# Kernel optimization log

Measured on AMD Instinct MI355X. Metric: run time of the kernel, lower is better.

## Reference

```python
import jax, jax.numpy as jnp
import numpy as np

B, N, K = 8, 2048, 16
C_IN, C_MID, C_OUT = 64, 16, 64
WH = [32, 32]
FH = [256]


def _mlp_params(key, dims, scale_keyed=True):
    ps = []
    for i in range(len(dims) - 1):
        key, k1 = jax.random.split(key)
        w = jax.random.normal(k1, (dims[i], dims[i + 1]), jnp.float32) / np.sqrt(dims[i])
        b = jnp.zeros((dims[i + 1],), jnp.float32)
        ps += [w, b]
    return ps


def setup_inputs() -> dict:
    key = jax.random.key(0)
    k1, k2, k3, k4, k5 = jax.random.split(key, 5)
    groups = jnp.broadcast_to(jnp.arange(N, dtype=jnp.int32) // K, (B, N))
    points = jax.random.normal(k1, (B, N, 3), jnp.float32)
    feats = jax.random.normal(k2, (B, N, C_IN), jnp.float32)
    point_mask = (jax.random.uniform(k3, (B, N)) > 0.1).astype(jnp.float32)
    w1, b1, w2, b2, w3, b3 = _mlp_params(k4, [3] + WH + [C_MID])
    f1, fb1, f2, fb2 = _mlp_params(k5, [C_IN * C_MID] + FH + [C_OUT])
    return {"groups": groups, "points": points, "feats": feats,
            "point_mask": point_mask,
            "w1": w1, "b1": b1, "w2": w2, "b2": b2, "w3": w3, "b3": b3,
            "f1": f1, "fb1": fb1, "f2": f2, "fb2": fb2}


def _neighbor_idxs(groups):
    # matches[b,i,j] = groups[b,i]==groups[b,j]; torch .nonzero yields, per (b,i),
    # the matching j in increasing order -> stable argsort of ~matches, take first K.
    matches = groups[:, :, None] == groups[:, None, :]            # [B,N,N]
    return jnp.argsort((~matches).astype(jnp.int32), axis=-1)[:, :, :K]  # [B,N,K]


def reference(groups, points, feats, point_mask,
              w1, b1, w2, b2, w3, b3, f1, fb1, f2, fb2):
    idxs = _neighbor_idxs(groups)                                  # [B,N,K] int
    gather = jax.vmap(lambda arr, ix: arr[ix])                     # per-batch gather
    nb_pts = gather(points, idxs)                                  # [B,N,K,3]
    nb_feats = gather(feats, idxs)                                 # [B,N,K,C_IN]
    rel = points[:, :, None, :] - nb_pts                           # [B,N,K,3] (xy encoding = identity)

    # weight_conv: pointwise MLP 3 -> 32 -> 32 -> C_MID, then explicit ReLU
    h = jax.nn.relu(rel @ w1 + b1)
    h = jax.nn.relu(h @ w2 + b2)
    m = jax.nn.relu(h @ w3 + b3)                                   # [B,N,K,C_MID]

    tmask = gather(point_mask, idxs)                               # [B,N,K]
    m = m * tmask[..., None]
    nb_feats = nb_feats * tmask[..., None]

    # per-(point) matmul: [C_MID,K] x [K,C_IN] -> flatten C_MID-major
    e = jnp.einsum('bnkm,bnkc->bnmc', m, nb_feats)                 # [B,N,C_MID,C_IN]
    e = e.reshape(B, N, C_MID * C_IN)

    # final_conv: pointwise MLP 1024 -> 256 -> C_OUT
    h2 = jax.nn.relu(e @ f1 + fb1)
    out = h2 @ f2 + fb2                                            # [B,N,C_OUT]
    return out
```

## Files before the change

kernel.cpp:

```cpp
#include <hip/hip_runtime.h>

typedef unsigned short u16;
typedef short bf16x8 __attribute__((ext_vector_type(8)));
typedef float f32x4  __attribute__((ext_vector_type(4)));
typedef u16   u16x4  __attribute__((ext_vector_type(4)));

__device__ __forceinline__ u16 f2bf(float f) {
  union { float f; unsigned int i; } v; v.f = f;
  unsigned int r = (v.i + 0x7FFFu + ((v.i >> 16) & 1u)) >> 16;
  return (u16)r;
}

__global__ __launch_bounds__(256) void repack_k(const float* __restrict__ f1,
                                                const float* __restrict__ f2,
                                                u16* __restrict__ f1p,
                                                u16* __restrict__ f2p) {
  const int o = blockIdx.x * 256 + threadIdx.x;
  if (o < 262144) {
    const int j = o & 7, n = (o >> 3) & 255, kb = o >> 11;
    f1p[o] = f2bf(f1[(kb * 8 + j) * 256 + n]);
  }
  if (o < 16384) {
    const int j = o & 7, n = (o >> 3) & 63, kb = o >> 9;
    f2p[o] = f2bf(f2[(kb * 8 + j) * 64 + n]);
  }
}

__global__ __launch_bounds__(256) void fused_k(
    const float* __restrict__ points, const float* __restrict__ feats,
    const float* __restrict__ pmask,
    const float* __restrict__ w1, const float* __restrict__ b1,
    const float* __restrict__ w2, const float* __restrict__ b2,
    const float* __restrict__ w3, const float* __restrict__ b3,
    const u16* __restrict__ f1p, const float* __restrict__ fb1,
    const u16* __restrict__ f2p, const float* __restrict__ fb2,
    float* __restrict__ out) {
  const int gi = blockIdx.x;
  const int bb = blockIdx.y;
  const int base = gi * 16;
  const int t = threadIdx.x;

  __shared__ float Wl[1712];
  __shared__ float Pl[16][3];
  __shared__ float Mask[16];
  __shared__ float F[1024];
  __shared__ __align__(16) u16 E[16 * 1032];
  __shared__ __align__(16) union {
    float Ml[16 * 16 * 17];
    u16   H2[16 * 264];
  } U;

  for (int idx = t; idx < 96;   idx += 256) Wl[idx]        = w1[idx];
  for (int idx = t; idx < 32;   idx += 256) Wl[96 + idx]   = b1[idx];
  for (int idx = t; idx < 1024; idx += 256) Wl[128 + idx]  = w2[idx];
  for (int idx = t; idx < 32;   idx += 256) Wl[1152 + idx] = b2[idx];
  for (int idx = t; idx < 512;  idx += 256) Wl[1184 + idx] = w3[idx];
  for (int idx = t; idx < 16;   idx += 256) Wl[1696 + idx] = b3[idx];
  if (t < 16) {
    Mask[t] = pmask[bb * 2048 + base + t];
    const int p = (bb * 2048 + base + t) * 3;
    Pl[t][0] = points[p + 0];
    Pl[t][1] = points[p + 1];
    Pl[t][2] = points[p + 2];
  }
  __syncthreads();

  for (int e = t; e < 1024; e += 256) {
    const int k = e >> 6;
    F[e] = feats[(bb * 2048 + base) * 64 + e] * Mask[k];
  }
  {
    const int i = t >> 4, k = t & 15;
    const float r0 = Pl[i][0] - Pl[k][0];
    const float r1 = Pl[i][1] - Pl[k][1];
    const float r2 = Pl[i][2] - Pl[k][2];
    float h1[32];
#pragma unroll
    for (int o = 0; o < 32; ++o) {
      float a = Wl[96 + o];
      a = fmaf(r0, Wl[o], a);
      a = fmaf(r1, Wl[32 + o], a);
      a = fmaf(r2, Wl[64 + o], a);
      h1[o] = fmaxf(a, 0.f);
    }
    float h2[32];
#pragma unroll
    for (int o = 0; o < 32; ++o) h2[o] = Wl[1152 + o];
#pragma unroll
    for (int j = 0; j < 32; ++j) {
      const float hj = h1[j];
      const float* w = &Wl[128 + j * 32];
#pragma unroll
      for (int o = 0; o < 32; ++o) h2[o] = fmaf(hj, w[o], h2[o]);
    }
#pragma unroll
    for (int o = 0; o < 32; ++o) h2[o] = fmaxf(h2[o], 0.f);
    float mo[16];
#pragma unroll
    for (int o = 0; o < 16; ++o) mo[o] = Wl[1696 + o];
#pragma unroll
    for (int j = 0; j < 32; ++j) {
      const float hj = h2[j];
      const float* w = &Wl[1184 + j * 16];
#pragma unroll
      for (int o = 0; o < 16; ++o) mo[o] = fmaf(hj, w[o], mo[o]);
    }
    const float mk = Mask[k];
    float* Mrow = &U.Ml[(i * 16 + k) * 17];
#pragma unroll
    for (int o = 0; o < 16; ++o) Mrow[o] = fmaxf(mo[o], 0.f) * mk;
  }
  __syncthreads();

  {
    const int i = t >> 4;
    const int c0 = (t & 15) * 4;
    float acc[16][4] = {};
#pragma unroll
    for (int k = 0; k < 16; ++k) {
      const float* Fr = &F[k * 64 + c0];
      const float f0 = Fr[0], fA = Fr[1], fB = Fr[2], fC = Fr[3];
      const float* Mrow = &U.Ml[(i * 16 + k) * 17];
#pragma unroll
      for (int mi = 0; mi < 16; ++mi) {
        const float mv = Mrow[mi];
        acc[mi][0] = fmaf(mv, f0, acc[mi][0]);
        acc[mi][1] = fmaf(mv, fA, acc[mi][1]);
        acc[mi][2] = fmaf(mv, fB, acc[mi][2]);
        acc[mi][3] = fmaf(mv, fC, acc[mi][3]);
      }
    }
    __syncthreads();
#pragma unroll
    for (int mi = 0; mi < 16; ++mi) {
      u16x4 v = { f2bf(acc[mi][0]), f2bf(acc[mi][1]), f2bf(acc[mi][2]), f2bf(acc[mi][3]) };
      *(u16x4*)&E[i * 1032 + mi * 64 + c0] = v;
    }
  }
  __syncthreads();

  {
    const int wv = t >> 6;
    const int lane = t & 63;
    const int q = lane >> 4, r16 = lane & 15;
    const int nb = wv * 64;
    f32x4 acc[4] = {};
    for (int ks = 0; ks < 32; ++ks) {
      const int k0 = ks * 32;
      const bf16x8 a = *(const bf16x8*)&E[r16 * 1032 + k0 + q * 8];
      const int kb = (k0 >> 3) + q;
#pragma unroll
      for (int nt = 0; nt < 4; ++nt) {
        const bf16x8 bv = *(const bf16x8*)&f1p[(kb * 256 + nb + nt * 16 + r16) * 8];
        acc[nt] = __builtin_amdgcn_mfma_f32_16x16x32_bf16(a, bv, acc[nt], 0, 0, 0);
      }
    }
    __syncthreads();
#pragma unroll
    for (int nt = 0; nt < 4; ++nt) {
      const int col = nb + nt * 16 + r16;
      const float bias = fb1[col];
#pragma unroll
      for (int r = 0; r < 4; ++r)
        U.H2[(q * 4 + r) * 264 + col] = f2bf(fmaxf(acc[nt][r] + bias, 0.f));
    }
  }
  __syncthreads();

  {
    const int wv = t >> 6;
    const int lane = t & 63;
    const int q = lane >> 4, r16 = lane & 15;
    const int n0 = wv * 16;
    f32x4 acc = {};
#pragma unroll
    for (int ks = 0; ks < 8; ++ks) {
      const int k0 = ks * 32;
      const bf16x8 a = *(const bf16x8*)&U.H2[r16 * 264 + k0 + q * 8];
      const bf16x8 bv = *(const bf16x8*)&f2p[(((k0 >> 3) + q) * 64 + n0 + r16) * 8];
      acc = __builtin_amdgcn_mfma_f32_16x16x32_bf16(a, bv, acc, 0, 0, 0);
    }
    const int col = n0 + r16;
    const float bias = fb2[col];
#pragma unroll
    for (int r = 0; r < 4; ++r) {
      const int row = q * 4 + r;
      out[((size_t)(bb * 2048 + base + row)) * 64 + col] = acc[r] + bias;
    }
  }
}

extern "C" void kernel_launch(void* const* d_in, const int* in_sizes, int n_in,
                              void* d_out, int out_size, void* d_ws, size_t ws_size,
                              hipStream_t stream) {
  const float* points = (const float*)d_in[1];
  const float* feats  = (const float*)d_in[2];
  const float* pmask  = (const float*)d_in[3];
  const float* w1 = (const float*)d_in[4];
  const float* b1 = (const float*)d_in[5];
  const float* w2 = (const float*)d_in[6];
  const float* b2 = (const float*)d_in[7];
  const float* w3 = (const float*)d_in[8];
  const float* b3 = (const float*)d_in[9];
  const float* f1 = (const float*)d_in[10];
  const float* fb1 = (const float*)d_in[11];
  const float* f2 = (const float*)d_in[12];
  const float* fb2 = (const float*)d_in[13];
  float* out = (float*)d_out;

  u16* f1p = (u16*)d_ws;
  u16* f2p = f1p + 262144;

  repack_k<<<dim3(1024), dim3(256), 0, stream>>>(f1, f2, f1p, f2p);
  fused_k<<<dim3(128, 8), dim3(256), 0, stream>>>(points, feats, pmask,
                                                  w1, b1, w2, b2, w3, b3,
                                                  f1p, fb1, f2p, fb2, out);
}
```

Baseline: 131.7 us.

## Split fused kernel into MLP/einsum stage and tiled double-buffered GEMM

Splits the work into two kernels. The first runs the weight MLP and the einsum, writes E to a global bf16 workspace, and folds in the f1/f2 repacking. The second is a 64-row-tile GEMM that double-buffers A tiles into LDS with XOR swizzling via global_load_lds, then applies the second layer. The aim is more reuse of the f1 weights per block (64 rows instead of 16) and overlapping loads with MFMA, at the cost of a 32MB round trip through global memory for E. It falls back to the old path when the workspace is too small.

```diff
diff --git a/kernel.cpp b/kernel.cpp
--- a/kernel.cpp
+++ b/kernel.cpp
@@ -25,6 +25,227 @@
     f2p[o] = f2bf(f2[(kb * 8 + j) * 64 + n]);
   }
 }
+
+__global__ __launch_bounds__(256) void mlp_einsum_k(
+    const float* __restrict__ points, const float* __restrict__ feats,
+    const float* __restrict__ pmask,
+    const float* __restrict__ w1, const float* __restrict__ b1,
+    const float* __restrict__ w2, const float* __restrict__ b2,
+    const float* __restrict__ w3, const float* __restrict__ b3,
+    const float* __restrict__ f1, const float* __restrict__ f2,
+    u16* __restrict__ f1p, u16* __restrict__ f2p,
+    u16* __restrict__ Eg) {
+  const int gi = blockIdx.x;
+  const int bb = blockIdx.y;
+  const int base = gi * 16;
+  const int t = threadIdx.x;
+
+  __shared__ float Wl[1712];
+  __shared__ float Pl[16][3];
+  __shared__ float Mask[16];
+  __shared__ float F[1024];
+  __shared__ float Ml[16 * 16 * 17];
+
+  {
+    const int o = (bb * 128 + gi) * 256 + t;
+    { const int j = o & 7, n = (o >> 3) & 255, kb = o >> 11;
+      f1p[o] = f2bf(f1[(kb * 8 + j) * 256 + n]); }
+    if (o < 16384) {
+      const int j = o & 7, n = (o >> 3) & 63, kb = o >> 9;
+      f2p[o] = f2bf(f2[(kb * 8 + j) * 64 + n]);
+    }
+  }
+
+  for (int idx = t; idx < 96;   idx += 256) Wl[idx]        = w1[idx];
+  for (int idx = t; idx < 32;   idx += 256) Wl[96 + idx]   = b1[idx];
+  for (int idx = t; idx < 1024; idx += 256) Wl[128 + idx]  = w2[idx];
+  for (int idx = t; idx < 32;   idx += 256) Wl[1152 + idx] = b2[idx];
+  for (int idx = t; idx < 512;  idx += 256) Wl[1184 + idx] = w3[idx];
+  for (int idx = t; idx < 16;   idx += 256) Wl[1696 + idx] = b3[idx];
+  if (t < 16) {
+    Mask[t] = pmask[bb * 2048 + base + t];
+    const int p = (bb * 2048 + base + t) * 3;
+    Pl[t][0] = points[p + 0];
+    Pl[t][1] = points[p + 1];
+    Pl[t][2] = points[p + 2];
+  }
+  __syncthreads();
+
+  for (int e = t; e < 1024; e += 256) {
+    const int k = e >> 6;
+    F[e] = feats[(bb * 2048 + base) * 64 + e] * Mask[k];
+  }
+  {
+    const int i = t >> 4, k = t & 15;
+    const float r0 = Pl[i][0] - Pl[k][0];
+    const float r1 = Pl[i][1] - Pl[k][1];
+    const float r2 = Pl[i][2] - Pl[k][2];
+    float h1[32];
+#pragma unroll
+    for (int o = 0; o < 32; ++o) {
+      float a = Wl[96 + o];
+      a = fmaf(r0, Wl[o], a);
+      a = fmaf(r1, Wl[32 + o], a);
+      a = fmaf(r2, Wl[64 + o], a);
+      h1[o] = fmaxf(a, 0.f);
+    }
+    float h2[32];
+#pragma unroll
+    for (int o = 0; o < 32; ++o) h2[o] = Wl[1152 + o];
+#pragma unroll
+    for (int j = 0; j < 32; ++j) {
+      const float hj = h1[j];
+      const float* w = &Wl[128 + j * 32];
+#pragma unroll
+      for (int o = 0; o < 32; ++o) h2[o] = fmaf(hj, w[o], h2[o]);
+    }
+#pragma unroll
+    for (int o = 0; o < 32; ++o) h2[o] = fmaxf(h2[o], 0.f);
+    float mo[16];
+#pragma unroll
+    for (int o = 0; o < 16; ++o) mo[o] = Wl[1696 + o];
+#pragma unroll
+    for (int j = 0; j < 32; ++j) {
+      const float hj = h2[j];
+      const float* w = &Wl[1184 + j * 16];
+#pragma unroll
+      for (int o = 0; o < 16; ++o) mo[o] = fmaf(hj, w[o], mo[o]);
+    }
+    const float mk = Mask[k];
+    float* Mrow = &Ml[(i * 16 + k) * 17];
+#pragma unroll
+    for (int o = 0; o < 16; ++o) Mrow[o] = fmaxf(mo[o], 0.f) * mk;
+  }
+  __syncthreads();
+
+  {
+    const int i = t >> 4;
+    const int c0 = (t & 15) * 4;
+    float acc[16][4] = {};
+#pragma unroll
+    for (int k = 0; k < 16; ++k) {
+      const float* Fr = &F[k * 64 + c0];
+      const float f0 = Fr[0], fA = Fr[1], fB = Fr[2], fC = Fr[3];
+      const float* Mrow = &Ml[(i * 16 + k) * 17];
+#pragma unroll
+      for (int mi = 0; mi < 16; ++mi) {
+        const float mv = Mrow[mi];
+        acc[mi][0] = fmaf(mv, f0, acc[mi][0]);
+        acc[mi][1] = fmaf(mv, fA, acc[mi][1]);
+        acc[mi][2] = fmaf(mv, fB, acc[mi][2]);
+        acc[mi][3] = fmaf(mv, fC, acc[mi][3]);
+      }
+    }
+    u16* Erow = Eg + (size_t)(bb * 2048 + base + i) * 1024;
+#pragma unroll
+    for (int mi = 0; mi < 16; ++mi) {
+      u16x4 v = { f2bf(acc[mi][0]), f2bf(acc[mi][1]),
+                  f2bf(acc[mi][2]), f2bf(acc[mi][3]) };
+      *(u16x4*)&Erow[mi * 64 + c0] = v;
+    }
+  }
+}
+
+#define STAGE(bf_, kc_)                                                        \
+  do {                                                                         \
+    const int rl_ = lane >> 3;                                       \
+    const int sg_ = (lane & 7) ^ rl_;         \
+    const u16* s0_ =                                                           \
+        Eg + (size_t)(R + wv * 8 + rl_) * 1024 + (kc_) + sg_ * 8;              \
+    u16* d0_ = &Asw[bf_][(wv * 8) * 64];            \
+    u16* d1_ = &Asw[bf_][(32 + wv * 8) * 64];                                  \
+    __builtin_amdgcn_global_load_lds(                                          \
+        (const __attribute__((address_space(1))) void*)s0_,                    \
+        (__attribute__((address_space(3))) void*)d0_, 16, 0, 0);               \
+    __builtin_amdgcn_global_load_lds(                                          \
+        (const __attribute__((address_space(1))) void*)(s0_ + 32 * 1024),      \
+        (__attribute__((address_space(3))) void*)d1_, 16, 0, 0);               \
+  } while (0)
+
+__global__ __launch_bounds__(256) void gemm_k(
+    const u16* __restrict__ Eg, const u16* __restrict__ f1p,
+    const float* __restrict__ fb1, const u16* __restrict__ f2p,
+    const float* __restrict__ fb2, float* __restrict__ out) {
+  const int R = blockIdx.x * 64;
+  const int t = threadIdx.x;
+  const int wv = t >> 6, lane = t & 63;
+  const int q = lane >> 4, r16 = lane & 15;
+
+  __shared__ __align__(16) u16 Asw[2][64 * 64];
+  __shared__ __align__(16) u16 H2[64 * 264];
+
+  const int nb = wv * 64;
+  f32x4 acc[4][4] = {};
+
+  STAGE(0, 0);
+  for (int c = 0; c < 16; ++c) {
+    const int bf = c & 1;
+    asm volatile("s_waitcnt vmcnt(0)" ::: "memory");
+    __builtin_amdgcn_s_barrier();
+
+    bf16x8 bv[2][4];
+#pragma unroll
+    for (int ksl = 0; ksl < 2; ++ksl) {
+      const int kb = c * 8 + ksl * 4 + q;
+#pragma unroll
+      for (int nt = 0; nt < 4; ++nt)
+        bv[ksl][nt] =
+            *(const bf16x8*)&f1p[(size_t)(kb * 256 + nb + nt * 16 + r16) * 8];
+    }
+    bf16x8 a[2][4];
+#pragma unroll
+    for (int ksl = 0; ksl < 2; ++ksl)
+#pragma unroll
+      for (int rt = 0; rt < 4; ++rt) {
+        const int r = rt * 16 + r16;
+        const int g = (ksl * 4 + q) ^ (r & 7);
+        a[ksl][rt] = *(const bf16x8*)&Asw[bf][r * 64 + g * 8];
+      }
+    __builtin_amdgcn_sched_barrier(0);
+    if (c < 15) STAGE(bf ^ 1, (c + 1) * 64);
+    __builtin_amdgcn_sched_barrier(0);
+#pragma unroll
+    for (int ksl = 0; ksl < 2; ++ksl)
+#pragma unroll
+      for (int nt = 0; nt < 4; ++nt)
+#pragma unroll
+        for (int rt = 0; rt < 4; ++rt)
+          acc[rt][nt] = __builtin_amdgcn_mfma_f32_16x16x32_bf16(
+              a[ksl][rt], bv[ksl][nt], acc[rt][nt], 0, 0, 0);
+    __builtin_amdgcn_s_barrier();
+  }
+
+#pragma unroll
+  for (int nt = 0; nt < 4; ++nt) {
+    const int col = nb + nt * 16 + r16;
+    const float bias = fb1[col];
+#pragma unroll
+    for (int rt = 0; rt < 4; ++rt)
+#pragma unroll
+      for (int r = 0; r < 4; ++r)
+        H2[(rt * 16 + q * 4 + r) * 264 + col] =
+            f2bf(fmaxf(acc[rt][nt][r] + bias, 0.f));
+  }
+  __syncthreads();
+
+  const int n0 = wv * 16;
+  const float bias2 = fb2[n0 + r16];
+#pragma unroll
+  for (int rt = 0; rt < 4; ++rt) {
+    f32x4 a2 = {};
+#pragma unroll
+    for (int ks = 0; ks < 8; ++ks) {
+      const bf16x8 av = *(const bf16x8*)&H2[(rt * 16 + r16) * 264 + ks * 32 + q * 8];
+      const bf16x8 b2v =
+          *(const bf16x8*)&f2p[(size_t)((ks * 4 + q) * 64 + n0 + r16) * 8];
+      a2 = __builtin_amdgcn_mfma_f32_16x16x32_bf16(av, b2v, a2, 0, 0, 0);
+    }
+#pragma unroll
+    for (int r = 0; r < 4; ++r)
+      out[(size_t)(R + rt * 16 + q * 4 + r) * 64 + n0 + r16] = a2[r] + bias2;
+  }
+}
+#undef STAGE
 
 __global__ __launch_bounds__(256) void fused_k(
     const float* __restrict__ points, const float* __restrict__ feats,
@@ -151,8 +372,8 @@
       const int kb = (k0 >> 3) + q;
 #pragma unroll
       for (int nt = 0; nt < 4; ++nt) {
-        const bf16x8 bv = *(const bf16x8*)&f1p[(kb * 256 + nb + nt * 16 + r16) * 8];
-        acc[nt] = __builtin_amdgcn_mfma_f32_16x16x32_bf16(a, bv, acc[nt], 0, 0, 0);
+        const bf16x8 bvv = *(const bf16x8*)&f1p[(kb * 256 + nb + nt * 16 + r16) * 8];
+        acc[nt] = __builtin_amdgcn_mfma_f32_16x16x32_bf16(a, bvv, acc[nt], 0, 0, 0);
       }
     }
     __syncthreads();
@@ -177,8 +398,8 @@
     for (int ks = 0; ks < 8; ++ks) {
       const int k0 = ks * 32;
       const bf16x8 a = *(const bf16x8*)&U.H2[r16 * 264 + k0 + q * 8];
-      const bf16x8 bv = *(const bf16x8*)&f2p[(((k0 >> 3) + q) * 64 + n0 + r16) * 8];
-      acc = __builtin_amdgcn_mfma_f32_16x16x32_bf16(a, bv, acc, 0, 0, 0);
+      const bf16x8 bvv = *(const bf16x8*)&f2p[(((k0 >> 3) + q) * 64 + n0 + r16) * 8];
+      acc = __builtin_amdgcn_mfma_f32_16x16x32_bf16(a, bvv, acc, 0, 0, 0);
     }
     const int col = n0 + r16;
     const float bias = fb2[col];
@@ -210,9 +431,17 @@
 
   u16* f1p = (u16*)d_ws;
   u16* f2p = f1p + 262144;
-
-  repack_k<<<dim3(1024), dim3(256), 0, stream>>>(f1, f2, f1p, f2p);
-  fused_k<<<dim3(128, 8), dim3(256), 0, stream>>>(points, feats, pmask,
-                                                  w1, b1, w2, b2, w3, b3,
-                                                  f1p, fb1, f2p, fb2, out);
-}
+  const size_t NEED = 524288 + 32768 + (size_t)16384 * 1024 * 2;
+
+  if (ws_size >= NEED) {
+    u16* Eg = f2p + 16384;
+    mlp_einsum_k<<<dim3(128, 8), dim3(256), 0, stream>>>(
+        points, feats, pmask, w1, b1, w2, b2, w3, b3, f1, f2, f1p, f2p, Eg);
+    gemm_k<<<dim3(256), dim3(256), 0, stream>>>(Eg, f1p, fb1, f2p, fb2, out);
+  } else {
+    repack_k<<<dim3(1024), dim3(256), 0, stream>>>(f1, f2, f1p, f2p);
+    fused_k<<<dim3(128, 8), dim3(256), 0, stream>>>(points, feats, pmask,
+                                                    w1, b1, w2, b2, w3, b3,
+                                                    f1p, fb1, f2p, fb2, out);
+  }
+}
```

New measurement: 140.0 us. 6.3% more time.
